# Optimization experiments

Hardware: AMD Instinct MI355X
Metric: run time of the kernel (lower is better)

## Reference

```python
import jax, jax.numpy as jnp
import numpy as np

B, S, D, H = 2, 2048, 1024, 16
MASK_VAL = -50000.0

def setup_inputs() -> dict:
    key = jax.random.key(0)
    k1, k2, k3, k4 = jax.random.split(key, 4)
    # weights stored as [in, out] so projection is x @ W (equals torch Linear with W.T)
    s = 1.0 / np.sqrt(D)
    return {
        "x": jax.random.normal(k1, (B, S, D), dtype=jnp.float32),
        "Wq": jax.random.normal(k2, (D, D), dtype=jnp.float32) * s,
        "Wkv": jax.random.normal(k3, (D, 2 * D), dtype=jnp.float32) * s,
        "Wo": jax.random.normal(k4, (D, D), dtype=jnp.float32) * s,
    }

def reference(x, Wq, Wkv, Wo):
    b, sl, d = x.shape
    h = H
    hd = d // h
    scale = hd ** (-0.5)
    q = x @ Wq                      # [b, sl, d]
    kv = x @ Wkv                    # [b, sl, 2d]
    k, v = jnp.split(kv, 2, axis=-1)
    # [b, h, s, hd]
    q = q.reshape(b, sl, h, hd).transpose(0, 2, 1, 3)
    k = k.reshape(b, sl, h, hd).transpose(0, 2, 1, 3)
    v = v.reshape(b, sl, h, hd).transpose(0, 2, 1, 3)
    dots = jnp.einsum('bhid,bhjd->bhij', q * scale, k)  # [b,h,s,s]
    # causal: strictly-upper-triangular entries set to MASK_VAL
    causal = jnp.tril(jnp.ones((sl, sl), dtype=bool))
    dots = jnp.where(causal, dots, MASK_VAL)
    attn = jax.nn.softmax(dots, axis=-1)
    out = jnp.einsum('bhij,bhjd->bihd', attn, v).reshape(b, sl, d)
    return out @ Wo
```

## Files before the change

kernel.cpp:

```cpp
#include <hip/hip_runtime.h>

typedef __bf16 bf16_t;
typedef unsigned short u16;
typedef __attribute__((ext_vector_type(8))) __bf16 bf16x8;
typedef __attribute__((ext_vector_type(4))) float f32x4;
typedef __attribute__((ext_vector_type(4))) u16 u16x4;
typedef __attribute__((ext_vector_type(8))) u16 u16x8;

#define SS 2048

__device__ __forceinline__ u16 f2b(float f) {
    return __builtin_bit_cast(u16, (__bf16)f);
}

__device__ __forceinline__ float fexp2(float x) {
#if __has_builtin(__builtin_amdgcn_exp2f)
    return __builtin_amdgcn_exp2f(x);
#else
    float r;
    asm("v_exp_f32 %0, %1" : "=v"(r) : "v"(x));
    return r;
#endif
}

__device__ __forceinline__ void async_copy16(const u16* g, u16* l) {
    __builtin_amdgcn_global_load_lds(
        (__attribute__((address_space(1))) void*)(u16*)g,
        (__attribute__((address_space(3))) void*)l, 16, 0, 0);
}

__device__ __forceinline__ bf16x8 ldfrag(const u16* p) {
    return __builtin_bit_cast(bf16x8, *(const u16x8*)p);
}

__global__ __launch_bounds__(256)
void cast_x_kernel(const float* __restrict__ x, u16* __restrict__ xb) {
    size_t i = ((size_t)blockIdx.x * 256 + threadIdx.x) * 8;
    float4 a = *(const float4*)(x + i);
    float4 b = *(const float4*)(x + i + 4);
    u16x8 o;
    o[0] = f2b(a.x); o[1] = f2b(a.y); o[2] = f2b(a.z); o[3] = f2b(a.w);
    o[4] = f2b(b.x); o[5] = f2b(b.y); o[6] = f2b(b.z); o[7] = f2b(b.w);
    *(u16x8*)(xb + i) = o;
}

__global__ __launch_bounds__(256)
void transpose_all(const float* __restrict__ Wq, const float* __restrict__ Wkv,
                   const float* __restrict__ Wo, u16* __restrict__ WcatT,
                   u16* __restrict__ WoT) {
    const int z = blockIdx.z;
    if (z != 1 && blockIdx.y >= 16) return;
    const float* src; u16* dst; int N; float scale;
    if (z == 0)      { src = Wq;  dst = WcatT;               N = 1024; scale = 0.125f * 1.44269504089f; }
    else if (z == 1) { src = Wkv; dst = WcatT + 1024 * 1024; N = 2048; scale = 1.0f; }
    else             { src = Wo;  dst = WoT;                 N = 1024; scale = 1.0f; }
    __shared__ __attribute__((aligned(16))) u16 tile[64][72];
    const int k0 = blockIdx.x * 64, n0 = blockIdx.y * 64;
    const int tid = threadIdx.x;
#pragma unroll
    for (int p = 0; p < 4; ++p) {
        int c = p * 256 + tid;
        int r = c >> 4, c4 = c & 15;
        float4 v = *(const float4*)(src + (size_t)(k0 + r) * N + n0 + c4 * 4);
        u16x4 o;
        o[0] = f2b(v.x * scale); o[1] = f2b(v.y * scale);
        o[2] = f2b(v.z * scale); o[3] = f2b(v.w * scale);
        *(u16x4*)&tile[r][c4 * 4] = o;
    }
    __syncthreads();
#pragma unroll
    for (int p = 0; p < 4; ++p) {
        int c = p * 256 + tid;
        int n = c >> 4, k4 = c & 15;
        u16x4 o;
#pragma unroll
        for (int i = 0; i < 4; ++i) o[i] = tile[k4 * 4 + i][n];
        *(u16x4*)(dst + (size_t)(n0 + n) * 1024 + k0 + k4 * 4) = o;
    }
}

__global__ __launch_bounds__(256)
void transpose_v(const u16* __restrict__ QKV, u16* __restrict__ VTg) {
    __shared__ __attribute__((aligned(16))) u16 tile[64][72];
    const int s0 = blockIdx.x * 64;
    const int bh = blockIdx.y;
    const int b = bh >> 4, h = bh & 15;
    const int tid = threadIdx.x;
    const u16* src = QKV + ((size_t)b * SS + s0) * 3072 + 2048 + h * 64;
#pragma unroll
    for (int p = 0; p < 4; ++p) {
        int c = p * 256 + tid;
        int s = c >> 4, h4 = c & 15;
        *(u16x4*)&tile[s][h4 * 4] = *(const u16x4*)(src + (size_t)s * 3072 + h4 * 4);
    }
    __syncthreads();
    u16* dst = VTg + (size_t)bh * 64 * 2048 + s0;
#pragma unroll
    for (int p = 0; p < 4; ++p) {
        int c = p * 256 + tid;
        int hd = c >> 4, s4 = c & 15;
        u16x4 o;
#pragma unroll
        for (int i = 0; i < 4; ++i) o[i] = tile[s4 * 4 + i][hd];
        const int sb = s4 * 4;
        const int col = (sb & 32) | ((sb & 12) << 1) | ((sb >> 2) & 4);
        *(u16x4*)(dst + (size_t)hd * 2048 + col) = o;
    }
}

template <typename OutT>
__global__ __launch_bounds__(256, 3)
void gemm_bt(const u16* __restrict__ A, const u16* __restrict__ BT,
             OutT* __restrict__ C, int M, int N, int K) {
    __shared__ __attribute__((aligned(16))) u16 As[2][128 * 32];
    __shared__ __attribute__((aligned(16))) u16 Bs[2][128 * 32];
    const int tid = threadIdx.x;
    const int wave = tid >> 6, lane = tid & 63;
    const int l15 = lane & 15, quad = lane >> 4;
    const int m0 = blockIdx.y * 128, n0 = blockIdx.x * 128;
    const int wm = (wave >> 1) * 64, wn = (wave & 1) * 64;
    const f32x4 zero = {0.f, 0.f, 0.f, 0.f};
    f32x4 acc[4][4];
#pragma unroll
    for (int i = 0; i < 4; ++i)
#pragma unroll
        for (int j = 0; j < 4; ++j) acc[i][j] = zero;
    const int r0 = tid >> 2, kc = (tid & 3) * 8;
    auto stage = [&](int bsel, int k0) {
        async_copy16(A + (size_t)(m0 + r0) * K + k0 + kc, As[bsel] + tid * 8);
        async_copy16(BT + (size_t)(n0 + r0) * K + k0 + kc, Bs[bsel] + tid * 8);
        async_copy16(A + (size_t)(m0 + 64 + r0) * K + k0 + kc, As[bsel] + (256 + tid) * 8);
        async_copy16(BT + (size_t)(n0 + 64 + r0) * K + k0 + kc, Bs[bsel] + (256 + tid) * 8);
    };
    stage(0, 0);
    __syncthreads();
    const int nk = K >> 5;
    for (int t = 0; t < nk; ++t) {
        if (t + 1 < nk) stage((t + 1) & 1, (t + 1) * 32);
        const u16* Ab = As[t & 1];
        const u16* Bb = Bs[t & 1];
        bf16x8 af[4], bf[4];
#pragma unroll
        for (int s = 0; s < 4; ++s) {
            af[s] = ldfrag(Ab + (wm + s * 16 + l15) * 32 + quad * 8);
            bf[s] = ldfrag(Bb + (wn + s * 16 + l15) * 32 + quad * 8);
        }
#pragma unroll
        for (int mt = 0; mt < 4; ++mt)
#pragma unroll
            for (int nt = 0; nt < 4; ++nt)
                acc[mt][nt] = __builtin_amdgcn_mfma_f32_16x16x32_bf16(
                    af[mt], bf[nt], acc[mt][nt], 0, 0, 0);
        __syncthreads();
    }
#pragma unroll
    for (int mt = 0; mt < 4; ++mt)
#pragma unroll
        for (int nt = 0; nt < 4; ++nt) {
            const int n = n0 + wn + nt * 16 + l15;
#pragma unroll
            for (int r = 0; r < 4; ++r) {
                const int m = m0 + wm + mt * 16 + quad * 4 + r;
                float v = acc[mt][nt][r];
                if constexpr (sizeof(OutT) == 2) C[(size_t)m * N + n] = (OutT)f2b(v);
                else                             C[(size_t)m * N + n] = v;
            }
        }
}

__global__ __launch_bounds__(256, 2)
void gemm_bt64(const u16* __restrict__ A, const u16* __restrict__ BT,
               float* __restrict__ C, int M, int N, int K) {
    __shared__ __attribute__((aligned(16))) u16 As[2][128 * 32];
    __shared__ __attribute__((aligned(16))) u16 Bs[2][64 * 32];
    const int tid = threadIdx.x;
    const int wave = tid >> 6, lane = tid & 63;
    const int l15 = lane & 15, quad = lane >> 4;
    const int m0 = blockIdx.y * 128, n0 = blockIdx.x * 64;
    const int wm = (wave >> 1) * 64, wn = (wave & 1) * 32;
    const f32x4 zero = {0.f, 0.f, 0.f, 0.f};
    f32x4 acc[4][2];
#pragma unroll
    for (int i = 0; i < 4; ++i)
#pragma unroll
        for (int j = 0; j < 2; ++j) acc[i][j] = zero;
    const int r0 = tid >> 2, kc = (tid & 3) * 8;
    auto stage = [&](int bsel, int k0) {
        async_copy16(A + (size_t)(m0 + r0) * K + k0 + kc, As[bsel] + tid * 8);
        async_copy16(A + (size_t)(m0 + 64 + r0) * K + k0 + kc, As[bsel] + (256 + tid) * 8);
        async_copy16(BT + (size_t)(n0 + r0) * K + k0 + kc, Bs[bsel] + tid * 8);
    };
    stage(0, 0);
    __syncthreads();
    const int nk = K >> 5;
    for (int t = 0; t < nk; ++t) {
        if (t + 1 < nk) stage((t + 1) & 1, (t + 1) * 32);
        const u16* Ab = As[t & 1];
        const u16* Bb = Bs[t & 1];
        bf16x8 af[4], bf[2];
#pragma unroll
        for (int s = 0; s < 4; ++s)
            af[s] = ldfrag(Ab + (wm + s * 16 + l15) * 32 + quad * 8);
#pragma unroll
        for (int s = 0; s < 2; ++s)
            bf[s] = ldfrag(Bb + (wn + s * 16 + l15) * 32 + quad * 8);
#pragma unroll
        for (int mt = 0; mt < 4; ++mt)
#pragma unroll
            for (int nt = 0; nt < 2; ++nt)
                acc[mt][nt] = __builtin_amdgcn_mfma_f32_16x16x32_bf16(
                    af[mt], bf[nt], acc[mt][nt], 0, 0, 0);
        __syncthreads();
    }
#pragma unroll
    for (int mt = 0; mt < 4; ++mt)
#pragma unroll
        for (int nt = 0; nt < 2; ++nt) {
            const int n = n0 + wn + nt * 16 + l15;
#pragma unroll
            for (int r = 0; r < 4; ++r) {
                const int m = m0 + wm + mt * 16 + quad * 4 + r;
                C[(size_t)m * N + n] = acc[mt][nt][r];
            }
        }
}

__global__ __launch_bounds__(256, 2)
void attn_kernel(const u16* __restrict__ QKV, const u16* __restrict__ VTg,
                 u16* __restrict__ AO) {
    __shared__ __attribute__((aligned(16))) u16 Kt[2][2 * 64 * 32];
    __shared__ __attribute__((aligned(16))) u16 Vt[2][2 * 64 * 32];
    const int tid = threadIdx.x;
    const int wave = tid >> 6, lane = tid & 63;
    const int l15 = lane & 15, quad = lane >> 4;
    const int w16 = wave * 16;
    const int bh = blockIdx.y, b = bh >> 4, h = bh & 15;
    const int xe = b ? 15 - (int)blockIdx.x : (int)blockIdx.x;
    const int qbA = 31 - xe, qbB = xe;
    const int qA0 = qbA * 64, qB0 = qbB * 64;
    const size_t bS = (size_t)b * SS;
    const u16* vbase = VTg + (size_t)bh * 64 * 2048;
    const int rr = (tid >> 2) & 63, kc8 = (tid & 3) * 8;

    {
        const u16* ksrc = QKV + (bS + rr) * 3072 + 1024 + h * 64 + kc8;
        async_copy16(ksrc,      Kt[0] + tid * 8);
        async_copy16(ksrc + 32, Kt[0] + (256 + tid) * 8);
        const u16* vsrc = vbase + (size_t)rr * 2048 + kc8;
        async_copy16(vsrc,      Vt[0] + tid * 8);
        async_copy16(vsrc + 32, Vt[0] + (256 + tid) * 8);
    }
    bf16x8 qfA[2], qfB[2];
    {
        const u16* qA = QKV + (bS + qA0 + w16 + l15) * 3072 + h * 64 + quad * 8;
        qfA[0] = ldfrag(qA); qfA[1] = ldfrag(qA + 32);
        const u16* qB = QKV + (bS + qB0 + w16 + l15) * 3072 + h * 64 + quad * 8;
        qfB[0] = ldfrag(qB); qfB[1] = ldfrag(qB + 32);
    }
    float lA = 0.f, lB = 0.f;
    f32x4 OA[4], OB[4];
    const f32x4 zero = {0.f, 0.f, 0.f, 0.f};
#pragma unroll
    for (int nt = 0; nt < 4; ++nt) { OA[nt] = zero; OB[nt] = zero; }
    const f32x4 cinit = {-10.f, -10.f, -10.f, -10.f};
    __syncthreads();

    for (int j = 0; j <= qbA; ++j) {
        if (j < qbA) {
            const int kv1 = (j + 1) * 64;
            const int nb = (j + 1) & 1;
            const u16* ksrc = QKV + (bS + kv1 + rr) * 3072 + 1024 + h * 64 + kc8;
            async_copy16(ksrc,      Kt[nb] + tid * 8);
            async_copy16(ksrc + 32, Kt[nb] + (256 + tid) * 8);
            const u16* vsrc = vbase + (size_t)rr * 2048 + kv1 + kc8;
            async_copy16(vsrc,      Vt[nb] + tid * 8);
            async_copy16(vsrc + 32, Vt[nb] + (256 + tid) * 8);
        }
        const bool bAct = (j <= qbB);
        const bool dA = (j == qbA), dB = (j == qbB);
        const u16* KB = Kt[j & 1];
        const u16* VB = Vt[j & 1];
        bf16x8 vf[4][2];
#pragma unroll
        for (int nt = 0; nt < 4; ++nt)
#pragma unroll
            for (int ks = 0; ks < 2; ++ks)
                vf[nt][ks] = ldfrag(VB + ks * 2048 + (nt * 16 + l15) * 32 + quad * 8);
        u16x4 pcA[4], pcB[4];
#pragma unroll
        for (int c = 0; c < 4; ++c) {
            bf16x8 kf0 = ldfrag(KB + (c * 16 + l15) * 32 + quad * 8);
            bf16x8 kf1 = ldfrag(KB + 2048 + (c * 16 + l15) * 32 + quad * 8);
            f32x4 a = __builtin_amdgcn_mfma_f32_16x16x32_bf16(kf0, qfA[0], cinit, 0, 0, 0);
            f32x4 s = __builtin_amdgcn_mfma_f32_16x16x32_bf16(kf1, qfA[1], a, 0, 0, 0);
            if (dA) {
#pragma unroll
                for (int r = 0; r < 4; ++r)
                    if (c * 16 + quad * 4 + r > w16 + l15) s[r] = -1e30f;
            }
            u16x4 pk; float acc = 0.f;
#pragma unroll
            for (int r = 0; r < 4; ++r) {
                float pv = fexp2(s[r]);
                acc += pv;
                pk[r] = f2b(pv);
            }
            lA += acc; pcA[c] = pk;
            if (bAct) {
                f32x4 a2 = __builtin_amdgcn_mfma_f32_16x16x32_bf16(kf0, qfB[0], cinit, 0, 0, 0);
                f32x4 s2 = __builtin_amdgcn_mfma_f32_16x16x32_bf16(kf1, qfB[1], a2, 0, 0, 0);
                if (dB) {
#pragma unroll
                    for (int r = 0; r < 4; ++r)
                        if (c * 16 + quad * 4 + r > w16 + l15) s2[r] = -1e30f;
                }
                u16x4 pk2; float acc2 = 0.f;
#pragma unroll
                for (int r = 0; r < 4; ++r) {
                    float pv = fexp2(s2[r]);
                    acc2 += pv;
                    pk2[r] = f2b(pv);
                }
                lB += acc2; pcB[c] = pk2;
            }
        }
        bf16x8 paA[2], paB[2];
#pragma unroll
        for (int ks = 0; ks < 2; ++ks) {
            u16x8 t;
#pragma unroll
            for (int i = 0; i < 4; ++i) { t[i] = pcA[2 * ks][i]; t[4 + i] = pcA[2 * ks + 1][i]; }
            paA[ks] = __builtin_bit_cast(bf16x8, t);
        }
#pragma unroll
        for (int nt = 0; nt < 4; ++nt) {
            OA[nt] = __builtin_amdgcn_mfma_f32_16x16x32_bf16(paA[0], vf[nt][0], OA[nt], 0, 0, 0);
            OA[nt] = __builtin_amdgcn_mfma_f32_16x16x32_bf16(paA[1], vf[nt][1], OA[nt], 0, 0, 0);
        }
        if (bAct) {
#pragma unroll
            for (int ks = 0; ks < 2; ++ks) {
                u16x8 t;
#pragma unroll
                for (int i = 0; i < 4; ++i) { t[i] = pcB[2 * ks][i]; t[4 + i] = pcB[2 * ks + 1][i]; }
                paB[ks] = __builtin_bit_cast(bf16x8, t);
            }
#pragma unroll
            for (int nt = 0; nt < 4; ++nt) {
                OB[nt] = __builtin_amdgcn_mfma_f32_16x16x32_bf16(paB[0], vf[nt][0], OB[nt], 0, 0, 0);
                OB[nt] = __builtin_amdgcn_mfma_f32_16x16x32_bf16(paB[1], vf[nt][1], OB[nt], 0, 0, 0);
            }
        }
        __syncthreads();
    }

    lA += __shfl_xor(lA, 16); lA += __shfl_xor(lA, 32);
    lB += __shfl_xor(lB, 16); lB += __shfl_xor(lB, 32);
#pragma unroll
    for (int r = 0; r < 4; ++r) {
        const int ql = quad * 4 + r;
        float invA = 1.0f / __shfl(lA, ql);
        float invB = 1.0f / __shfl(lB, ql);
        size_t rowA = bS + (size_t)qA0 + w16 + ql;
        size_t rowB = bS + (size_t)qB0 + w16 + ql;
#pragma unroll
        for (int nt = 0; nt < 4; ++nt) {
            AO[rowA * 1024 + h * 64 + nt * 16 + l15] = f2b(OA[nt][r] * invA);
            AO[rowB * 1024 + h * 64 + nt * 16 + l15] = f2b(OB[nt][r] * invB);
        }
    }
}

extern "C" void kernel_launch(void* const* d_in, const int* in_sizes, int n_in,
                              void* d_out, int out_size, void* d_ws, size_t ws_size,
                              hipStream_t stream) {
    (void)in_sizes; (void)n_in; (void)out_size; (void)ws_size;
    const float* x   = (const float*)d_in[0];
    const float* Wq  = (const float*)d_in[1];
    const float* Wkv = (const float*)d_in[2];
    const float* Wo  = (const float*)d_in[3];
    float* out = (float*)d_out;
    char* ws = (char*)d_ws;
    u16* xb    = (u16*)(ws);
    u16* WcatT = (u16*)(ws + (size_t)(8 << 20));
    u16* WoT   = (u16*)(ws + (size_t)(14 << 20));
    u16* QKV   = (u16*)(ws + (size_t)(16 << 20));
    u16* VTb   = (u16*)(ws + (size_t)(40 << 20));
    u16* AO    = xb;

    cast_x_kernel<<<2048, 256, 0, stream>>>(x, xb);
    transpose_all<<<dim3(16, 32, 3), 256, 0, stream>>>(Wq, Wkv, Wo, WcatT, WoT);
    gemm_bt<u16><<<dim3(24, 32), 256, 0, stream>>>(xb, WcatT, QKV, 4096, 3072, 1024);
    transpose_v<<<dim3(32, 32), 256, 0, stream>>>(QKV, VTb);
    attn_kernel<<<dim3(16, 32), 256, 0, stream>>>(QKV, VTb, AO);
    gemm_bt64<<<dim3(16, 32), 256, 0, stream>>>(AO, WoT, out, 4096, 1024, 1024);
}
```

Before: 183.2 us.

## Split paired causal query blocks into one query block per workgroup

The attention kernel previously had each workgroup handle two query blocks (a long and a short one, paired for load balance) that shared the K/V tiles. Now each workgroup handles a single query block, the grid doubles to 32x32, and launch bounds rise to 4 blocks per CU. This roughly halves register pressure and raises occupancy and the number of independent workgroups. In exchange, K/V tiles are loaded once per query block instead of being shared by two, and the work per workgroup becomes unbalanced, relying on the descending block order to schedule long blocks first.

```diff
diff --git a/kernel.cpp b/kernel.cpp
--- a/kernel.cpp
+++ b/kernel.cpp
@@ -225,7 +225,7 @@
         }
 }
 
-__global__ __launch_bounds__(256, 2)
+__global__ __launch_bounds__(256, 4)
 void attn_kernel(const u16* __restrict__ QKV, const u16* __restrict__ VTg,
                  u16* __restrict__ AO) {
     __shared__ __attribute__((aligned(16))) u16 Kt[2][2 * 64 * 32];
@@ -235,9 +235,8 @@
     const int l15 = lane & 15, quad = lane >> 4;
     const int w16 = wave * 16;
     const int bh = blockIdx.y, b = bh >> 4, h = bh & 15;
-    const int xe = b ? 15 - (int)blockIdx.x : (int)blockIdx.x;
-    const int qbA = 31 - xe, qbB = xe;
-    const int qA0 = qbA * 64, qB0 = qbB * 64;
+    const int qb = 31 - (int)blockIdx.x;
+    const int q0 = qb * 64;
     const size_t bS = (size_t)b * SS;
     const u16* vbase = VTg + (size_t)bh * 64 * 2048;
     const int rr = (tid >> 2) & 63, kc8 = (tid & 3) * 8;
@@ -250,23 +249,21 @@
         async_copy16(vsrc,      Vt[0] + tid * 8);
         async_copy16(vsrc + 32, Vt[0] + (256 + tid) * 8);
     }
-    bf16x8 qfA[2], qfB[2];
+    bf16x8 qf[2];
     {
-        const u16* qA = QKV + (bS + qA0 + w16 + l15) * 3072 + h * 64 + quad * 8;
-        qfA[0] = ldfrag(qA); qfA[1] = ldfrag(qA + 32);
-        const u16* qB = QKV + (bS + qB0 + w16 + l15) * 3072 + h * 64 + quad * 8;
-        qfB[0] = ldfrag(qB); qfB[1] = ldfrag(qB + 32);
-    }
-    float lA = 0.f, lB = 0.f;
-    f32x4 OA[4], OB[4];
+        const u16* q = QKV + (bS + q0 + w16 + l15) * 3072 + h * 64 + quad * 8;
+        qf[0] = ldfrag(q); qf[1] = ldfrag(q + 32);
+    }
+    float l_i = 0.f;
+    f32x4 O[4];
     const f32x4 zero = {0.f, 0.f, 0.f, 0.f};
 #pragma unroll
-    for (int nt = 0; nt < 4; ++nt) { OA[nt] = zero; OB[nt] = zero; }
+    for (int nt = 0; nt < 4; ++nt) O[nt] = zero;
     const f32x4 cinit = {-10.f, -10.f, -10.f, -10.f};
     __syncthreads();
 
-    for (int j = 0; j <= qbA; ++j) {
-        if (j < qbA) {
+    for (int j = 0; j <= qb; ++j) {
+        if (j < qb) {
             const int kv1 = (j + 1) * 64;
             const int nb = (j + 1) & 1;
             const u16* ksrc = QKV + (bS + kv1 + rr) * 3072 + 1024 + h * 64 + kc8;
@@ -276,8 +273,7 @@
             async_copy16(vsrc,      Vt[nb] + tid * 8);
             async_copy16(vsrc + 32, Vt[nb] + (256 + tid) * 8);
         }
-        const bool bAct = (j <= qbB);
-        const bool dA = (j == qbA), dB = (j == qbB);
+        const bool d = (j == qb);
         const u16* KB = Kt[j & 1];
         const u16* VB = Vt[j & 1];
         bf16x8 vf[4][2];
@@ -286,14 +282,14 @@
 #pragma unroll
             for (int ks = 0; ks < 2; ++ks)
                 vf[nt][ks] = ldfrag(VB + ks * 2048 + (nt * 16 + l15) * 32 + quad * 8);
-        u16x4 pcA[4], pcB[4];
+        u16x4 pc[4];
 #pragma unroll
         for (int c = 0; c < 4; ++c) {
             bf16x8 kf0 = ldfrag(KB + (c * 16 + l15) * 32 + quad * 8);
             bf16x8 kf1 = ldfrag(KB + 2048 + (c * 16 + l15) * 32 + quad * 8);
-            f32x4 a = __builtin_amdgcn_mfma_f32_16x16x32_bf16(kf0, qfA[0], cinit, 0, 0, 0);
-            f32x4 s = __builtin_amdgcn_mfma_f32_16x16x32_bf16(kf1, qfA[1], a, 0, 0, 0);
-            if (dA) {
+            f32x4 a = __builtin_amdgcn_mfma_f32_16x16x32_bf16(kf0, qf[0], cinit, 0, 0, 0);
+            f32x4 s = __builtin_amdgcn_mfma_f32_16x16x32_bf16(kf1, qf[1], a, 0, 0, 0);
+            if (d) {
 #pragma unroll
                 for (int r = 0; r < 4; ++r)
                     if (c * 16 + quad * 4 + r > w16 + l15) s[r] = -1e30f;
@@ -305,69 +301,33 @@
                 acc += pv;
                 pk[r] = f2b(pv);
             }
-            lA += acc; pcA[c] = pk;
-            if (bAct) {
-                f32x4 a2 = __builtin_amdgcn_mfma_f32_16x16x32_bf16(kf0, qfB[0], cinit, 0, 0, 0);
-                f32x4 s2 = __builtin_amdgcn_mfma_f32_16x16x32_bf16(kf1, qfB[1], a2, 0, 0, 0);
-                if (dB) {
-#pragma unroll
-                    for (int r = 0; r < 4; ++r)
-                        if (c * 16 + quad * 4 + r > w16 + l15) s2[r] = -1e30f;
-                }
-                u16x4 pk2; float acc2 = 0.f;
-#pragma unroll
-                for (int r = 0; r < 4; ++r) {
-                    float pv = fexp2(s2[r]);
-                    acc2 += pv;
-                    pk2[r] = f2b(pv);
-                }
-                lB += acc2; pcB[c] = pk2;
-            }
-        }
-        bf16x8 paA[2], paB[2];
+            l_i += acc; pc[c] = pk;
+        }
+        bf16x8 pa[2];
 #pragma unroll
         for (int ks = 0; ks < 2; ++ks) {
             u16x8 t;
 #pragma unroll
-            for (int i = 0; i < 4; ++i) { t[i] = pcA[2 * ks][i]; t[4 + i] = pcA[2 * ks + 1][i]; }
-            paA[ks] = __builtin_bit_cast(bf16x8, t);
+            for (int i = 0; i < 4; ++i) { t[i] = pc[2 * ks][i]; t[4 + i] = pc[2 * ks + 1][i]; }
+            pa[ks] = __builtin_bit_cast(bf16x8, t);
         }
 #pragma unroll
         for (int nt = 0; nt < 4; ++nt) {
-            OA[nt] = __builtin_amdgcn_mfma_f32_16x16x32_bf16(paA[0], vf[nt][0], OA[nt], 0, 0, 0);
-            OA[nt] = __builtin_amdgcn_mfma_f32_16x16x32_bf16(paA[1], vf[nt][1], OA[nt], 0, 0, 0);
-        }
-        if (bAct) {
-#pragma unroll
-            for (int ks = 0; ks < 2; ++ks) {
-                u16x8 t;
-#pragma unroll
-                for (int i = 0; i < 4; ++i) { t[i] = pcB[2 * ks][i]; t[4 + i] = pcB[2 * ks + 1][i]; }
-                paB[ks] = __builtin_bit_cast(bf16x8, t);
-            }
-#pragma unroll
-            for (int nt = 0; nt < 4; ++nt) {
-                OB[nt] = __builtin_amdgcn_mfma_f32_16x16x32_bf16(paB[0], vf[nt][0], OB[nt], 0, 0, 0);
-                OB[nt] = __builtin_amdgcn_mfma_f32_16x16x32_bf16(paB[1], vf[nt][1], OB[nt], 0, 0, 0);
-            }
+            O[nt] = __builtin_amdgcn_mfma_f32_16x16x32_bf16(pa[0], vf[nt][0], O[nt], 0, 0, 0);
+            O[nt] = __builtin_amdgcn_mfma_f32_16x16x32_bf16(pa[1], vf[nt][1], O[nt], 0, 0, 0);
         }
         __syncthreads();
     }
 
-    lA += __shfl_xor(lA, 16); lA += __shfl_xor(lA, 32);
-    lB += __shfl_xor(lB, 16); lB += __shfl_xor(lB, 32);
+    l_i += __shfl_xor(l_i, 16); l_i += __shfl_xor(l_i, 32);
 #pragma unroll
     for (int r = 0; r < 4; ++r) {
         const int ql = quad * 4 + r;
-        float invA = 1.0f / __shfl(lA, ql);
-        float invB = 1.0f / __shfl(lB, ql);
-        size_t rowA = bS + (size_t)qA0 + w16 + ql;
-        size_t rowB = bS + (size_t)qB0 + w16 + ql;
-#pragma unroll
-        for (int nt = 0; nt < 4; ++nt) {
-            AO[rowA * 1024 + h * 64 + nt * 16 + l15] = f2b(OA[nt][r] * invA);
-            AO[rowB * 1024 + h * 64 + nt * 16 + l15] = f2b(OB[nt][r] * invB);
-        }
+        float inv = 1.0f / __shfl(l_i, ql);
+        size_t row = bS + (size_t)q0 + w16 + ql;
+#pragma unroll
+        for (int nt = 0; nt < 4; ++nt)
+            AO[row * 1024 + h * 64 + nt * 16 + l15] = f2b(O[nt][r] * inv);
     }
 }
 
@@ -392,6 +352,6 @@
     transpose_all<<<dim3(16, 32, 3), 256, 0, stream>>>(Wq, Wkv, Wo, WcatT, WoT);
     gemm_bt<u16><<<dim3(24, 32), 256, 0, stream>>>(xb, WcatT, QKV, 4096, 3072, 1024);
     transpose_v<<<dim3(32, 32), 256, 0, stream>>>(QKV, VTb);
-    attn_kernel<<<dim3(16, 32), 256, 0, stream>>>(QKV, VTb, AO);
+    attn_kernel<<<dim3(32, 32), 256, 0, stream>>>(QKV, VTb, AO);
     gemm_bt64<<<dim3(16, 32), 256, 0, stream>>>(AO, WoT, out, 4096, 1024, 1024);
 }
```

After: 191.7 us. +4.7%, slower.
